# Kernel optimization log

Measured on AMD Instinct MI355X. Metric: run time of the kernel, lower is better.

The kernel has to match this reference:

```python
import jax, jax.numpy as jnp
import numpy as np

B, H, E, R, T = 2048, 512, 300, 512, 50


def setup_inputs() -> dict:
    key = jax.random.key(0)
    ks = jax.random.split(key, 12)
    s = 0.02  # xavier-ish scale for params
    return {
        "x": jax.random.normal(ks[0], (B, E), jnp.float32),
        "h_enc": jax.random.normal(ks[1], (B, R), jnp.float32),
        "phi_history": jax.random.normal(ks[2], (T, B, H), jnp.float32),
        "cell_history": jax.random.normal(ks[3], (T, B, H), jnp.float32),
        "h_summ": jax.random.normal(ks[4], (B, H), jnp.float32),
        "c_summ": jax.random.normal(ks[5], (B, H), jnp.float32),
        "W_w": jax.random.normal(ks[6], (4 * H, H + E), jnp.float32) * s,
        "W_b": jnp.zeros((4 * H,), jnp.float32),
        "v_w": jax.random.normal(ks[7], (1, H), jnp.float32) * s,
        "v_b": jnp.zeros((1,), jnp.float32),
        "lq_w": jax.random.normal(ks[8], (H, R), jnp.float32) * s,
        "lq_b": jnp.zeros((H,), jnp.float32),
        "lk_w": jax.random.normal(ks[9], (H, H), jnp.float32) * s,
        "lk_b": jnp.zeros((H,), jnp.float32),
        "ls_w": jax.random.normal(ks[10], (H, H), jnp.float32) * s,
        "ls_b": jnp.zeros((H,), jnp.float32),
    }


def reference(x, h_enc, phi_history, cell_history, h_summ, c_summ,
              W_w, W_b, v_w, v_b, lq_w, lq_b, lk_w, lk_b, ls_w, ls_b):
    Hd = h_summ.shape[-1]
    # [T,B,H] -> [B,T,H] (torch.stack(...).transpose(0,1))
    phi = jnp.transpose(phi_history, (1, 0, 2))
    cell = jnp.transpose(cell_history, (1, 0, 2))
    # additive attention over cached history
    q = h_enc @ lq_w.T + lq_b                       # [B,H]
    k = jnp.einsum('bth,ah->bta', phi, lk_w) + lk_b  # [B,T,H]
    su = h_summ @ ls_w.T + ls_b                     # [B,H]
    e = jnp.tanh(q[:, None, :] + k + su[:, None, :])
    scores = jnp.einsum('bth,oh->bto', e, v_w)[..., 0] + v_b[0]  # [B,T]
    p = jax.nn.softmax(scores, axis=-1)
    h_s = jnp.einsum('bt,bth->bh', p, phi)
    c_s = jnp.einsum('bt,bth->bh', p, cell)
    # fused LSTM gates on [h_summ, x]
    gates = jnp.concatenate([h_s, x], axis=1) @ W_w.T + W_b  # [B,4H]
    f_t = jax.nn.sigmoid(gates[:, :Hd])
    o_t = jax.nn.sigmoid(gates[:, Hd:2 * Hd])
    i_t = jax.nn.sigmoid(gates[:, 2 * Hd:3 * Hd])
    ch_t = jnp.tanh(gates[:, 3 * Hd:])
    c_ctrl = f_t * c_s + i_t * ch_t
    h_ctrl = o_t * jnp.tanh(c_ctrl)
    return h_ctrl
```

## Files before the change

kernel.cpp:

```cpp
#include <hip/hip_runtime.h>
#include <math.h>

#define Bm 2048
#define Hm 512
#define Em 300
#define Tm 50
#define KWm 812
#define KWp 832

typedef unsigned short u16;
typedef unsigned int u32;
typedef __attribute__((ext_vector_type(8))) short short8;
typedef __attribute__((ext_vector_type(8))) u16 ushort8v;
typedef __attribute__((ext_vector_type(4))) float f32x4;

__device__ __forceinline__ float sigmoidf_(float x) { return 1.f / (1.f + __expf(-x)); }
__device__ __forceinline__ float tanhfast(float x) { return 1.f - 2.f / (__expf(2.f * x) + 1.f); }

__device__ __forceinline__ u16 bfr(float x) {
    union { float f; u32 u; } c; c.f = x;
    u32 u = c.u;
    u += 0x7FFFu + ((u >> 16) & 1u);
    return (u16)(u >> 16);
}
__device__ __forceinline__ ushort8v cvt8(const float* __restrict__ p) {
    f32x4 v0 = *(const f32x4*)p;
    f32x4 v1 = *(const f32x4*)(p + 4);
    ushort8v r;
    r[0] = bfr(v0[0]); r[1] = bfr(v0[1]); r[2] = bfr(v0[2]); r[3] = bfr(v0[3]);
    r[4] = bfr(v1[0]); r[5] = bfr(v1[1]); r[6] = bfr(v1[2]); r[7] = bfr(v1[3]);
    return r;
}

__device__ __forceinline__ void gload16(const u16* g, u16* l) {
    __builtin_amdgcn_global_load_lds((const __attribute__((address_space(1))) void*)g,
                                     (__attribute__((address_space(3))) void*)l, 16, 0, 0);
}

__global__ __launch_bounds__(256) void k_pack_phi(
        const float* __restrict__ phi, u16* __restrict__ phib) {
    const size_t nvec = (size_t)Tm * Bm * 512 / 8;
    for (size_t i = (size_t)blockIdx.x * 256 + threadIdx.x; i < nvec;
         i += (size_t)gridDim.x * 256)
        *(ushort8v*)&phib[i * 8] = cvt8(phi + i * 8);
}

__global__ __launch_bounds__(256) void k_pack(
        const float* __restrict__ henc, const float* __restrict__ hsum,
        const float* __restrict__ lq, const float* __restrict__ ls,
        const float* __restrict__ Ww, const float* __restrict__ x,
        const float* __restrict__ lkw,
        const float* __restrict__ lqb, const float* __restrict__ lsb,
        const float* __restrict__ lkb,
        u16* __restrict__ Aq, u16* __restrict__ Wq,
        u16* __restrict__ Wg, u16* __restrict__ Xb, u16* __restrict__ lkwb,
        float* __restrict__ qbias) {
    const int job = blockIdx.y;
    const int r = blockIdx.x;
    const int tid = threadIdx.x;
    if (job == 0) {
        for (int c = tid; c < 1024; c += 256) {
            float v = (c < 512) ? henc[(size_t)r * 512 + c] : hsum[(size_t)r * 512 + (c - 512)];
            Aq[(size_t)r * 1024 + c] = bfr(v);
        }
    } else if (job == 1) {
        if (r < 512)
            for (int c = tid; c < 1024; c += 256) {
                float v = (c < 512) ? lq[(size_t)r * 512 + c] : ls[(size_t)r * 512 + (c - 512)];
                Wq[(size_t)r * 1024 + c] = bfr(v);
            }
    } else if (job == 2) {
        for (int c = tid; c < KWp; c += 256)
            Wg[(size_t)r * KWp + c] = (c < KWm) ? bfr(Ww[(size_t)r * KWm + c]) : (u16)0;
    } else if (job == 3) {
        for (int c = 512 + tid; c < KWp; c += 256)
            Xb[(size_t)r * KWp + c] = (c < KWm) ? bfr(x[(size_t)r * Em + (c - 512)]) : (u16)0;
    } else if (job == 4) {
        if (r < 512)
            for (int c = tid; c < 512; c += 256)
                lkwb[(size_t)r * 512 + c] = bfr(lkw[(size_t)r * 512 + c]);
    } else {
        if (r == 0)
            for (int c = tid; c < 512; c += 256)
                qbias[c] = lqb[c] + lsb[c] + lkb[c];
    }
}

__global__ __launch_bounds__(256) void k_qs_mfma(
        const u16* __restrict__ Aq, const u16* __restrict__ Wq,
        float* __restrict__ qs) {
    __shared__ u16 Asl[64 * 32];
    __shared__ u16 Bsl[64 * 32];
    const int m0 = blockIdx.x * 64, n0 = blockIdx.y * 64;
    const int kbase = blockIdx.z * 512;
    const int tid = threadIdx.x, lane = tid & 63, wid = tid >> 6;
    const int wr = wid >> 1, wc = wid & 1;
    const int l15 = lane & 15, l4 = lane >> 4;
    const int srow = (wid << 4) + (lane >> 2);
    const int gchunk = (lane & 3) ^ ((srow >> 1) & 3);
    f32x4 acc[2][2];
    #pragma unroll
    for (int i = 0; i < 2; ++i)
        #pragma unroll
        for (int j = 0; j < 2; ++j) acc[i][j] = (f32x4){0.f, 0.f, 0.f, 0.f};

    for (int k0 = kbase; k0 < kbase + 512; k0 += 32) {
        __syncthreads();
        gload16(Aq + (size_t)(m0 + srow) * 1024 + k0 + gchunk * 8, &Asl[wid * 512]);
        gload16(Wq + (size_t)(n0 + srow) * 1024 + k0 + gchunk * 8, &Bsl[wid * 512]);
        __syncthreads();
        short8 af[2], bf[2];
        #pragma unroll
        for (int mf = 0; mf < 2; ++mf) {
            int r = wr * 32 + mf * 16 + l15;
            af[mf] = *(const short8*)&Asl[r * 32 + (l4 ^ ((r >> 1) & 3)) * 8];
        }
        #pragma unroll
        for (int nf = 0; nf < 2; ++nf) {
            int r = wc * 32 + nf * 16 + l15;
            bf[nf] = *(const short8*)&Bsl[r * 32 + (l4 ^ ((r >> 1) & 3)) * 8];
        }
        #pragma unroll
        for (int mf = 0; mf < 2; ++mf)
            #pragma unroll
            for (int nf = 0; nf < 2; ++nf)
                acc[mf][nf] = __builtin_amdgcn_mfma_f32_16x16x32_bf16(
                                  af[mf], bf[nf], acc[mf][nf], 0, 0, 0);
    }
    #pragma unroll
    for (int mf = 0; mf < 2; ++mf)
        #pragma unroll
        for (int nf = 0; nf < 2; ++nf)
            #pragma unroll
            for (int reg = 0; reg < 4; ++reg) {
                int b = m0 + wr * 32 + mf * 16 + l4 * 4 + reg;
                int h = n0 + wc * 32 + nf * 16 + l15;
                atomicAdd(&qs[(size_t)b * Hm + h], acc[mf][nf][reg]);
            }
}

__global__ __launch_bounds__(256) void k_scores_mfma(
        const u16* __restrict__ phib, const u16* __restrict__ lkwb,
        const float* __restrict__ qs2, const float* __restrict__ vw,
        const float* __restrict__ qbias, float* __restrict__ scores) {
    __shared__ u16 Asl[128 * 64];
    __shared__ u16 Bsl[128 * 64];
    const int d  = blockIdx.x;
    const int wg = (d & 7) * 400 + (d >> 3);
    const int n0 = (wg & 3) << 7;
    const int m0 = (wg >> 2) << 7;
    const int t  = m0 >> 11;
    const int b0 = m0 & (Bm - 1);
    const int tid = threadIdx.x, lane = tid & 63, wid = tid >> 6;
    const int wr = wid >> 1, wc = wid & 1;
    const int l15 = lane & 15, l4 = lane >> 4;
    const int srow_in = lane >> 3;
    const int schunk  = (lane & 7) ^ srow_in;

    f32x4 acc[4][4];
    #pragma unroll
    for (int i = 0; i < 4; ++i)
        #pragma unroll
        for (int j = 0; j < 4; ++j) acc[i][j] = (f32x4){0.f, 0.f, 0.f, 0.f};

    for (int kt = 0; kt < 8; ++kt) {
        const int k0 = kt << 6;
        __syncthreads();
        #pragma unroll
        for (int j = 0; j < 4; ++j) {
            int r = (wid << 5) + (j << 3) + srow_in;
            gload16(phib + (size_t)(m0 + r) * 512 + k0 + schunk * 8,
                    &Asl[((wid << 5) + (j << 3)) * 64]);
            gload16(lkwb + (size_t)(n0 + r) * 512 + k0 + schunk * 8,
                    &Bsl[((wid << 5) + (j << 3)) * 64]);
        }
        __syncthreads();
        short8 af[4][2], bf[4][2];
        #pragma unroll
        for (int mf = 0; mf < 4; ++mf) {
            int r = wr * 64 + mf * 16 + l15;
            #pragma unroll
            for (int ks = 0; ks < 2; ++ks) {
                int c = ks * 4 + l4;
                af[mf][ks] = *(const short8*)&Asl[r * 64 + (c ^ (r & 7)) * 8];
            }
        }
        #pragma unroll
        for (int nf = 0; nf < 4; ++nf) {
            int r = wc * 64 + nf * 16 + l15;
            #pragma unroll
            for (int ks = 0; ks < 2; ++ks) {
                int c = ks * 4 + l4;
                bf[nf][ks] = *(const short8*)&Bsl[r * 64 + (c ^ (r & 7)) * 8];
            }
        }
        __builtin_amdgcn_s_setprio(1);
        #pragma unroll
        for (int ks = 0; ks < 2; ++ks)
            #pragma unroll
            for (int mf = 0; mf < 4; ++mf)
                #pragma unroll
                for (int nf = 0; nf < 4; ++nf)
                    acc[mf][nf] = __builtin_amdgcn_mfma_f32_16x16x32_bf16(
                                      af[mf][ks], bf[nf][ks], acc[mf][nf], 0, 0, 0);
        __builtin_amdgcn_s_setprio(0);
    }

    float vws[4], qb[4];
    int av[4];
    #pragma unroll
    for (int nf = 0; nf < 4; ++nf) {
        av[nf] = n0 + wc * 64 + nf * 16 + l15;
        vws[nf] = vw[av[nf]];
        qb[nf]  = qbias[av[nf]];
    }
    #pragma unroll
    for (int mf = 0; mf < 4; ++mf) {
        #pragma unroll
        for (int reg = 0; reg < 4; ++reg) {
            int b = b0 + wr * 64 + mf * 16 + l4 * 4 + reg;
            const float* q = qs2 + (size_t)b * Hm;
            float s = 0.f;
            #pragma unroll
            for (int nf = 0; nf < 4; ++nf)
                s = fmaf(tanhfast(acc[mf][nf][reg] + q[av[nf]] + qb[nf]), vws[nf], s);
            #pragma unroll
            for (int o = 1; o < 16; o <<= 1) s += __shfl_xor(s, o);
            if (l15 == 0) atomicAdd(&scores[(size_t)b * Tm + t], s);
        }
    }
}

__global__ __launch_bounds__(256) void k_attn(
        const u16* __restrict__ phib, const float* __restrict__ cell,
        const float* __restrict__ scores,
        u16* __restrict__ Xb, float* __restrict__ cs) {
    __shared__ float p[Tm];
    const int b = blockIdx.x;
    const int tid = threadIdx.x;
    if (tid < 64) {
        float s = (tid < Tm) ? scores[(size_t)b * Tm + tid] : -INFINITY;
        float m = s;
        #pragma unroll
        for (int o = 32; o; o >>= 1) m = fmaxf(m, __shfl_xor(m, o));
        float ex = (tid < Tm) ? __expf(s - m) : 0.f;
        float sum = ex;
        #pragma unroll
        for (int o = 32; o; o >>= 1) sum += __shfl_xor(sum, o);
        if (tid < Tm) p[tid] = ex / sum;
    }
    __syncthreads();
    const int c0 = tid * 2;
    float ah0 = 0.f, ah1 = 0.f, ac0 = 0.f, ac1 = 0.f;
    for (int t = 0; t < Tm; ++t) {
        float w = p[t];
        const size_t rb = ((size_t)t * Bm + b) * 512 + c0;
        u32 ph2 = *(const u32*)&phib[rb];
        float2 ce2 = *(const float2*)&cell[rb];
        float p0 = __uint_as_float(ph2 << 16);
        float p1 = __uint_as_float(ph2 & 0xFFFF0000u);
        ah0 = fmaf(w, p0, ah0);
        ah1 = fmaf(w, p1, ah1);
        ac0 = fmaf(w, ce2.x, ac0);
        ac1 = fmaf(w, ce2.y, ac1);
    }
    *(u32*)&Xb[(size_t)b * KWp + c0] = (u32)bfr(ah0) | ((u32)bfr(ah1) << 16);
    *(float2*)&cs[(size_t)b * Hm + c0] = make_float2(ac0, ac1);
}

__global__ __launch_bounds__(256) void k_gates_mfma(
        const u16* __restrict__ Xb, const u16* __restrict__ Wg,
        float* __restrict__ gates) {
    __shared__ u16 Asl[64 * 32];
    __shared__ u16 Bsl[128 * 32];
    const int m0 = blockIdx.x * 64, n0 = blockIdx.y * 128;
    const int tid = threadIdx.x, lane = tid & 63, wid = tid >> 6;
    const int wr = wid >> 1, wc = wid & 1;
    const int l15 = lane & 15, l4 = lane >> 4;
    const int srow = (wid << 4) + (lane >> 2);
    const int gchunkA = (lane & 3) ^ ((srow >> 1) & 3);
    f32x4 acc[2][4];
    #pragma unroll
    for (int i = 0; i < 2; ++i)
        #pragma unroll
        for (int j = 0; j < 4; ++j) acc[i][j] = (f32x4){0.f, 0.f, 0.f, 0.f};

    for (int k0 = 0; k0 < KWp; k0 += 32) {
        __syncthreads();
        gload16(Xb + (size_t)(m0 + srow) * KWp + k0 + gchunkA * 8, &Asl[wid * 512]);
        #pragma unroll
        for (int j = 0; j < 2; ++j) {
            int brow = (wid << 5) + (j << 4) + (lane >> 2);
            int gchunkB = (lane & 3) ^ ((brow >> 1) & 3);
            gload16(Wg + (size_t)(n0 + brow) * KWp + k0 + gchunkB * 8,
                    &Bsl[wid * 1024 + j * 512]);
        }
        __syncthreads();
        short8 af[2], bf[4];
        #pragma unroll
        for (int mf = 0; mf < 2; ++mf) {
            int r = wr * 32 + mf * 16 + l15;
            af[mf] = *(const short8*)&Asl[r * 32 + (l4 ^ ((r >> 1) & 3)) * 8];
        }
        #pragma unroll
        for (int nf = 0; nf < 4; ++nf) {
            int r = wc * 64 + nf * 16 + l15;
            bf[nf] = *(const short8*)&Bsl[r * 32 + (l4 ^ ((r >> 1) & 3)) * 8];
        }
        #pragma unroll
        for (int mf = 0; mf < 2; ++mf)
            #pragma unroll
            for (int nf = 0; nf < 4; ++nf)
                acc[mf][nf] = __builtin_amdgcn_mfma_f32_16x16x32_bf16(
                                  af[mf], bf[nf], acc[mf][nf], 0, 0, 0);
    }
    #pragma unroll
    for (int mf = 0; mf < 2; ++mf)
        #pragma unroll
        for (int nf = 0; nf < 4; ++nf)
            #pragma unroll
            for (int reg = 0; reg < 4; ++reg) {
                int b = m0 + wr * 32 + mf * 16 + l4 * 4 + reg;
                int n = n0 + wc * 64 + nf * 16 + l15;
                gates[(size_t)b * 2048 + n] = acc[mf][nf][reg];
            }
}

__global__ __launch_bounds__(256) void k_lstm(
        const float* __restrict__ gates, const float* __restrict__ Wb,
        const float* __restrict__ cs, float* __restrict__ out) {
    const int idx = blockIdx.x * 256 + threadIdx.x;
    const int b = idx >> 9, h = idx & 511;
    const float* g = gates + (size_t)b * 2048;
    float f  = sigmoidf_(g[h]        + Wb[h]);
    float o  = sigmoidf_(g[512 + h]  + Wb[512 + h]);
    float ii = sigmoidf_(g[1024 + h] + Wb[1024 + h]);
    float ch = tanhfast( g[1536 + h] + Wb[1536 + h]);
    float c  = f * cs[idx] + ii * ch;
    out[idx] = o * tanhfast(c);
}

extern "C" void kernel_launch(void* const* d_in, const int* in_sizes, int n_in,
                              void* d_out, int out_size, void* d_ws, size_t ws_size,
                              hipStream_t stream) {
    const float* x      = (const float*)d_in[0];
    const float* h_enc  = (const float*)d_in[1];
    const float* phi    = (const float*)d_in[2];
    const float* cell   = (const float*)d_in[3];
    const float* h_summ = (const float*)d_in[4];
    const float* W_w    = (const float*)d_in[6];
    const float* W_b    = (const float*)d_in[7];
    const float* v_w    = (const float*)d_in[8];
    const float* lq_w   = (const float*)d_in[10];
    const float* lq_b   = (const float*)d_in[11];
    const float* lk_w   = (const float*)d_in[12];
    const float* lk_b   = (const float*)d_in[13];
    const float* ls_w   = (const float*)d_in[14];
    const float* ls_b   = (const float*)d_in[15];
    float* out = (float*)d_out;

    char* w = (char*)d_ws;
    u16*   phib   = (u16*)  (w);
    float* gates  = (float*)(w);
    float* qs     = (float*)(w + 104857600);
    float* scores = (float*)(w + 109051904);
    float* cs     = (float*)(w + 109461504);
    u16*   Aq     = (u16*)  (w + 113655808);
    u16*   Wq     = (u16*)  (w + 117850112);
    u16*   Wg     = (u16*)  (w + 118898688);
    u16*   Xb     = (u16*)  (w + 122306560);
    u16*   lkwb   = (u16*)  (w + 125714432);
    float* qbias  = (float*)(w + 126763008);

    hipMemsetAsync(qs, 0, 4194304 + (size_t)Bm * Tm * sizeof(float), stream);
    k_pack<<<dim3(2048, 6), 256, 0, stream>>>(h_enc, h_summ, lq_w, ls_w, W_w, x, lk_w,
                                              lq_b, ls_b, lk_b,
                                              Aq, Wq, Wg, Xb, lkwb, qbias);
    k_pack_phi<<<dim3(2048), 256, 0, stream>>>(phi, phib);
    k_qs_mfma<<<dim3(Bm / 64, Hm / 64, 2), 256, 0, stream>>>(Aq, Wq, qs);
    k_scores_mfma<<<dim3(3200), 256, 0, stream>>>(phib, lkwb, qs, v_w, qbias, scores);
    k_attn<<<dim3(Bm), 256, 0, stream>>>(phib, cell, scores, Xb, cs);
    k_gates_mfma<<<dim3(Bm / 64, 2048 / 128), 256, 0, stream>>>(Xb, Wg, gates);
    k_lstm<<<dim3((Bm * Hm) / 256), 256, 0, stream>>>(gates, W_b, cs, out);
}
```

Baseline: 312.4 us.

## Fuse prep kernels with q/s GEMM and retile gates GEMM with K=64

Merges the weight/activation packing, phi bf16 conversion and the q+s projection GEMM into one launch. The GEMM now converts fp32 to bf16 on the fly into LDS, so the Aq/Wq staging buffers go away. This removes two launches and one round trip through global memory. The gates GEMM switches to a 64-wide K tile with XOR swizzle, uses a swizzled 1D grid mapping for L2 locality, and raises wave priority around the MFMA block, so there are fewer barriers per FLOP. The tradeoff is that the fused prep kernel mixes heterogeneous jobs: the GEMM blocks now run concurrently with the bandwidth-heavy phi conversion and may contend with it.

```diff
diff --git a/kernel.cpp b/kernel.cpp
--- a/kernel.cpp
+++ b/kernel.cpp
@@ -37,106 +37,91 @@
                                      (__attribute__((address_space(3))) void*)l, 16, 0, 0);
 }
 
-__global__ __launch_bounds__(256) void k_pack_phi(
-        const float* __restrict__ phi, u16* __restrict__ phib) {
-    const size_t nvec = (size_t)Tm * Bm * 512 / 8;
-    for (size_t i = (size_t)blockIdx.x * 256 + threadIdx.x; i < nvec;
-         i += (size_t)gridDim.x * 256)
-        *(ushort8v*)&phib[i * 8] = cvt8(phi + i * 8);
-}
-
-__global__ __launch_bounds__(256) void k_pack(
+__global__ __launch_bounds__(256) void k_prep(
         const float* __restrict__ henc, const float* __restrict__ hsum,
         const float* __restrict__ lq, const float* __restrict__ ls,
         const float* __restrict__ Ww, const float* __restrict__ x,
         const float* __restrict__ lkw,
         const float* __restrict__ lqb, const float* __restrict__ lsb,
-        const float* __restrict__ lkb,
-        u16* __restrict__ Aq, u16* __restrict__ Wq,
+        const float* __restrict__ lkb, const float* __restrict__ phi,
         u16* __restrict__ Wg, u16* __restrict__ Xb, u16* __restrict__ lkwb,
-        float* __restrict__ qbias) {
+        float* __restrict__ qbias, u16* __restrict__ phib,
+        float* __restrict__ qs) {
     const int job = blockIdx.y;
     const int r = blockIdx.x;
     const int tid = threadIdx.x;
     if (job == 0) {
-        for (int c = tid; c < 1024; c += 256) {
-            float v = (c < 512) ? henc[(size_t)r * 512 + c] : hsum[(size_t)r * 512 + (c - 512)];
-            Aq[(size_t)r * 1024 + c] = bfr(v);
-        }
-    } else if (job == 1) {
-        if (r < 512)
-            for (int c = tid; c < 1024; c += 256) {
-                float v = (c < 512) ? lq[(size_t)r * 512 + c] : ls[(size_t)r * 512 + (c - 512)];
-                Wq[(size_t)r * 1024 + c] = bfr(v);
-            }
-    } else if (job == 2) {
         for (int c = tid; c < KWp; c += 256)
             Wg[(size_t)r * KWp + c] = (c < KWm) ? bfr(Ww[(size_t)r * KWm + c]) : (u16)0;
-    } else if (job == 3) {
+    } else if (job == 1) {
         for (int c = 512 + tid; c < KWp; c += 256)
             Xb[(size_t)r * KWp + c] = (c < KWm) ? bfr(x[(size_t)r * Em + (c - 512)]) : (u16)0;
-    } else if (job == 4) {
         if (r < 512)
             for (int c = tid; c < 512; c += 256)
                 lkwb[(size_t)r * 512 + c] = bfr(lkw[(size_t)r * 512 + c]);
-    } else {
         if (r == 0)
             for (int c = tid; c < 512; c += 256)
                 qbias[c] = lqb[c] + lsb[c] + lkb[c];
-    }
-}
-
-__global__ __launch_bounds__(256) void k_qs_mfma(
-        const u16* __restrict__ Aq, const u16* __restrict__ Wq,
-        float* __restrict__ qs) {
-    __shared__ u16 Asl[64 * 32];
-    __shared__ u16 Bsl[64 * 32];
-    const int m0 = blockIdx.x * 64, n0 = blockIdx.y * 64;
-    const int kbase = blockIdx.z * 512;
-    const int tid = threadIdx.x, lane = tid & 63, wid = tid >> 6;
-    const int wr = wid >> 1, wc = wid & 1;
-    const int l15 = lane & 15, l4 = lane >> 4;
-    const int srow = (wid << 4) + (lane >> 2);
-    const int gchunk = (lane & 3) ^ ((srow >> 1) & 3);
-    f32x4 acc[2][2];
-    #pragma unroll
-    for (int i = 0; i < 2; ++i)
-        #pragma unroll
-        for (int j = 0; j < 2; ++j) acc[i][j] = (f32x4){0.f, 0.f, 0.f, 0.f};
-
-    for (int k0 = kbase; k0 < kbase + 512; k0 += 32) {
-        __syncthreads();
-        gload16(Aq + (size_t)(m0 + srow) * 1024 + k0 + gchunk * 8, &Asl[wid * 512]);
-        gload16(Wq + (size_t)(n0 + srow) * 1024 + k0 + gchunk * 8, &Bsl[wid * 512]);
-        __syncthreads();
-        short8 af[2], bf[2];
-        #pragma unroll
-        for (int mf = 0; mf < 2; ++mf) {
-            int r = wr * 32 + mf * 16 + l15;
-            af[mf] = *(const short8*)&Asl[r * 32 + (l4 ^ ((r >> 1) & 3)) * 8];
-        }
-        #pragma unroll
-        for (int nf = 0; nf < 2; ++nf) {
-            int r = wc * 32 + nf * 16 + l15;
-            bf[nf] = *(const short8*)&Bsl[r * 32 + (l4 ^ ((r >> 1) & 3)) * 8];
+    } else if (job == 2) {
+        const size_t nvec = (size_t)Tm * Bm * 512 / 8;
+        for (size_t i = (size_t)r * 256 + tid; i < nvec; i += (size_t)2048 * 256)
+            *(ushort8v*)&phib[i * 8] = cvt8(phi + i * 8);
+    } else {
+        if (r >= 512) return;
+        __shared__ u16 Asl[64 * 32];
+        __shared__ u16 Bsl[64 * 32];
+        const int z = r & 1;
+        const int n0 = ((r >> 1) & 7) * 64;
+        const int m0 = (r >> 4) * 64;
+        const float* A = z ? hsum : henc;
+        const float* W = z ? ls : lq;
+        const int lane = tid & 63, wid = tid >> 6;
+        const int wr = wid >> 1, wc = wid & 1;
+        const int l15 = lane & 15, l4 = lane >> 4;
+        const int srow = tid >> 2;
+        const int gch  = tid & 3;
+        const int sslot = gch ^ ((srow >> 1) & 3);
+        f32x4 acc[2][2];
+        #pragma unroll
+        for (int i = 0; i < 2; ++i)
+            #pragma unroll
+            for (int j = 0; j < 2; ++j) acc[i][j] = (f32x4){0.f, 0.f, 0.f, 0.f};
+        for (int k0 = 0; k0 < 512; k0 += 32) {
+            __syncthreads();
+            *(ushort8v*)&Asl[srow * 32 + sslot * 8] =
+                cvt8(A + (size_t)(m0 + srow) * 512 + k0 + gch * 8);
+            *(ushort8v*)&Bsl[srow * 32 + sslot * 8] =
+                cvt8(W + (size_t)(n0 + srow) * 512 + k0 + gch * 8);
+            __syncthreads();
+            short8 af[2], bf[2];
+            #pragma unroll
+            for (int mf = 0; mf < 2; ++mf) {
+                int rr = wr * 32 + mf * 16 + l15;
+                af[mf] = *(const short8*)&Asl[rr * 32 + (l4 ^ ((rr >> 1) & 3)) * 8];
+            }
+            #pragma unroll
+            for (int nf = 0; nf < 2; ++nf) {
+                int rr = wc * 32 + nf * 16 + l15;
+                bf[nf] = *(const short8*)&Bsl[rr * 32 + (l4 ^ ((rr >> 1) & 3)) * 8];
+            }
+            #pragma unroll
+            for (int mf = 0; mf < 2; ++mf)
+                #pragma unroll
+                for (int nf = 0; nf < 2; ++nf)
+                    acc[mf][nf] = __builtin_amdgcn_mfma_f32_16x16x32_bf16(
+                                      af[mf], bf[nf], acc[mf][nf], 0, 0, 0);
         }
         #pragma unroll
         for (int mf = 0; mf < 2; ++mf)
             #pragma unroll
             for (int nf = 0; nf < 2; ++nf)
-                acc[mf][nf] = __builtin_amdgcn_mfma_f32_16x16x32_bf16(
-                                  af[mf], bf[nf], acc[mf][nf], 0, 0, 0);
-    }
-    #pragma unroll
-    for (int mf = 0; mf < 2; ++mf)
-        #pragma unroll
-        for (int nf = 0; nf < 2; ++nf)
-            #pragma unroll
-            for (int reg = 0; reg < 4; ++reg) {
-                int b = m0 + wr * 32 + mf * 16 + l4 * 4 + reg;
-                int h = n0 + wc * 32 + nf * 16 + l15;
-                atomicAdd(&qs[(size_t)b * Hm + h], acc[mf][nf][reg]);
-            }
+                #pragma unroll
+                for (int reg = 0; reg < 4; ++reg) {
+                    int b = m0 + wr * 32 + mf * 16 + l4 * 4 + reg;
+                    int h = n0 + wc * 32 + nf * 16 + l15;
+                    atomicAdd(&qs[(size_t)b * Hm + h], acc[mf][nf][reg]);
+                }
+    }
 }
 
 __global__ __launch_bounds__(256) void k_scores_mfma(
@@ -271,48 +256,68 @@
 __global__ __launch_bounds__(256) void k_gates_mfma(
         const u16* __restrict__ Xb, const u16* __restrict__ Wg,
         float* __restrict__ gates) {
-    __shared__ u16 Asl[64 * 32];
-    __shared__ u16 Bsl[128 * 32];
-    const int m0 = blockIdx.x * 64, n0 = blockIdx.y * 128;
+    __shared__ u16 Asl[64 * 64];
+    __shared__ u16 Bsl[128 * 64];
+    const int d  = blockIdx.x;
+    const int wg = (d & 7) * 64 + (d >> 3);
+    const int m0 = (wg & 31) << 6;
+    const int n0 = (wg >> 5) << 7;
     const int tid = threadIdx.x, lane = tid & 63, wid = tid >> 6;
     const int wr = wid >> 1, wc = wid & 1;
     const int l15 = lane & 15, l4 = lane >> 4;
-    const int srow = (wid << 4) + (lane >> 2);
-    const int gchunkA = (lane & 3) ^ ((srow >> 1) & 3);
+    const int rin = lane >> 3;
+    const int schunk = (lane & 7) ^ rin;
     f32x4 acc[2][4];
     #pragma unroll
     for (int i = 0; i < 2; ++i)
         #pragma unroll
         for (int j = 0; j < 4; ++j) acc[i][j] = (f32x4){0.f, 0.f, 0.f, 0.f};
 
-    for (int k0 = 0; k0 < KWp; k0 += 32) {
+    for (int kt = 0; kt < 13; ++kt) {
+        const int k0 = kt << 6;
         __syncthreads();
-        gload16(Xb + (size_t)(m0 + srow) * KWp + k0 + gchunkA * 8, &Asl[wid * 512]);
         #pragma unroll
         for (int j = 0; j < 2; ++j) {
-            int brow = (wid << 5) + (j << 4) + (lane >> 2);
-            int gchunkB = (lane & 3) ^ ((brow >> 1) & 3);
-            gload16(Wg + (size_t)(n0 + brow) * KWp + k0 + gchunkB * 8,
-                    &Bsl[wid * 1024 + j * 512]);
+            int r = (wid << 4) + (j << 3) + rin;
+            gload16(Xb + (size_t)(m0 + r) * KWp + k0 + schunk * 8,
+                    &Asl[((wid << 4) + (j << 3)) * 64]);
+        }
+        #pragma unroll
+        for (int j = 0; j < 4; ++j) {
+            int r = (wid << 5) + (j << 3) + rin;
+            gload16(Wg + (size_t)(n0 + r) * KWp + k0 + schunk * 8,
+                    &Bsl[((wid << 5) + (j << 3)) * 64]);
         }
         __syncthreads();
-        short8 af[2], bf[4];
+        short8 af[2][2], bf[4][2];
         #pragma unroll
         for (int mf = 0; mf < 2; ++mf) {
             int r = wr * 32 + mf * 16 + l15;
-            af[mf] = *(const short8*)&Asl[r * 32 + (l4 ^ ((r >> 1) & 3)) * 8];
+            #pragma unroll
+            for (int ks = 0; ks < 2; ++ks) {
+                int c = ks * 4 + l4;
+                af[mf][ks] = *(const short8*)&Asl[r * 64 + (c ^ (r & 7)) * 8];
+            }
         }
         #pragma unroll
         for (int nf = 0; nf < 4; ++nf) {
             int r = wc * 64 + nf * 16 + l15;
-            bf[nf] = *(const short8*)&Bsl[r * 32 + (l4 ^ ((r >> 1) & 3)) * 8];
-        }
-        #pragma unroll
-        for (int mf = 0; mf < 2; ++mf)
-            #pragma unroll
-            for (int nf = 0; nf < 4; ++nf)
-                acc[mf][nf] = __builtin_amdgcn_mfma_f32_16x16x32_bf16(
-                                  af[mf], bf[nf], acc[mf][nf], 0, 0, 0);
+            #pragma unroll
+            for (int ks = 0; ks < 2; ++ks) {
+                int c = ks * 4 + l4;
+                bf[nf][ks] = *(const short8*)&Bsl[r * 64 + (c ^ (r & 7)) * 8];
+            }
+        }
+        __builtin_amdgcn_s_setprio(1);
+        #pragma unroll
+        for (int ks = 0; ks < 2; ++ks)
+            #pragma unroll
+            for (int mf = 0; mf < 2; ++mf)
+                #pragma unroll
+                for (int nf = 0; nf < 4; ++nf)
+                    acc[mf][nf] = __builtin_amdgcn_mfma_f32_16x16x32_bf16(
+                                      af[mf][ks], bf[nf][ks], acc[mf][nf], 0, 0, 0);
+        __builtin_amdgcn_s_setprio(0);
     }
     #pragma unroll
     for (int mf = 0; mf < 2; ++mf)
@@ -365,21 +370,17 @@
     float* qs     = (float*)(w + 104857600);
     float* scores = (float*)(w + 109051904);
     float* cs     = (float*)(w + 109461504);
-    u16*   Aq     = (u16*)  (w + 113655808);
-    u16*   Wq     = (u16*)  (w + 117850112);
-    u16*   Wg     = (u16*)  (w + 118898688);
-    u16*   Xb     = (u16*)  (w + 122306560);
-    u16*   lkwb   = (u16*)  (w + 125714432);
-    float* qbias  = (float*)(w + 126763008);
+    u16*   Wg     = (u16*)  (w + 113655808);
+    u16*   Xb     = (u16*)  (w + 117063680);
+    u16*   lkwb   = (u16*)  (w + 120471552);
+    float* qbias  = (float*)(w + 121520128);
 
     hipMemsetAsync(qs, 0, 4194304 + (size_t)Bm * Tm * sizeof(float), stream);
-    k_pack<<<dim3(2048, 6), 256, 0, stream>>>(h_enc, h_summ, lq_w, ls_w, W_w, x, lk_w,
-                                              lq_b, ls_b, lk_b,
-                                              Aq, Wq, Wg, Xb, lkwb, qbias);
-    k_pack_phi<<<dim3(2048), 256, 0, stream>>>(phi, phib);
-    k_qs_mfma<<<dim3(Bm / 64, Hm / 64, 2), 256, 0, stream>>>(Aq, Wq, qs);
+    k_prep<<<dim3(2048, 4), 256, 0, stream>>>(h_enc, h_summ, lq_w, ls_w, W_w, x, lk_w,
+                                              lq_b, ls_b, lk_b, phi,
+                                              Wg, Xb, lkwb, qbias, phib, qs);
     k_scores_mfma<<<dim3(3200), 256, 0, stream>>>(phib, lkwb, qs, v_w, qbias, scores);
     k_attn<<<dim3(Bm), 256, 0, stream>>>(phib, cell, scores, Xb, cs);
-    k_gates_mfma<<<dim3(Bm / 64, 2048 / 128), 256, 0, stream>>>(Xb, Wg, gates);
+    k_gates_mfma<<<dim3(512), 256, 0, stream>>>(Xb, Wg, gates);
     k_lstm<<<dim3((Bm * Hm) / 256), 256, 0, stream>>>(gates, W_b, cs, out);
 }
```

New measurement: 308.5 us. No clear change (-1.2%).
